# Optimization experiments

Hardware: AMD Instinct MI355X
Metric: run time of the kernel (lower is better)

The kernel has to match this reference:

```python
import jax, jax.numpy as jnp
import numpy as np

WEIGHT = 2e-9       # lambda for the CRF loss
SIGMA_RGB = 15.0    # appearance (color) bandwidth
SIGMA_XY = 100.0    # spatial bandwidth (scaled by SCALE inside the loss, as in the torch module)
SCALE = 0.5         # scale_factor for both image and segmentation


def _nearest_resize(x, sf):
    # torch F.interpolate(mode='nearest'): src_idx = floor(dst_idx / sf)
    H, W = x.shape[-2:]
    Ho, Wo = int(H * sf), int(W * sf)
    iy = jnp.floor(jnp.arange(Ho) / sf).astype(jnp.int32)
    ix = jnp.floor(jnp.arange(Wo) / sf).astype(jnp.int32)
    return x[:, :, iy][:, :, :, ix]


def _bilinear_resize(x, sf):
    # torch F.interpolate(mode='bilinear', align_corners=False): src = (dst+0.5)/sf - 0.5
    N, C, H, W = x.shape
    Ho, Wo = int(H * sf), int(W * sf)

    def axis_idx(n_in, n_out):
        s = (jnp.arange(n_out, dtype=x.dtype) + 0.5) * (n_in / n_out) - 0.5
        s = jnp.clip(s, 0.0, n_in - 1)
        i0 = jnp.floor(s).astype(jnp.int32)
        i1 = jnp.minimum(i0 + 1, n_in - 1)
        w = (s - i0).astype(x.dtype)
        return i0, i1, w

    y0, y1, wy = axis_idx(H, Ho)
    x0, x1, wx = axis_idx(W, Wo)
    xr = x[:, :, y0, :] * (1.0 - wy)[None, None, :, None] + x[:, :, y1, :] * wy[None, None, :, None]
    return xr[:, :, :, x0] * (1.0 - wx) + xr[:, :, :, x1] * wx


def _dense_crf_loss(images, segmentations):
    img = _nearest_resize(images, SCALE)          # [N,3,H,W], values in [0,255]
    seg = _bilinear_resize(segmentations, SCALE)  # [N,K,H,W]
    N, Kc, H, W = seg.shape
    P = H * W
    sxy = SIGMA_XY * SCALE

    yy, xx = jnp.meshgrid(jnp.arange(H, dtype=img.dtype), jnp.arange(W, dtype=img.dtype), indexing='ij')
    pos = jnp.stack([xx, yy], 0) / sxy                       # [2,H,W]
    pos = jnp.broadcast_to(pos[None], (N, 2, H, W))
    feats = jnp.concatenate([pos, img / SIGMA_RGB], axis=1)  # [N,5,H,W]
    feats = feats.reshape(N, 5, P).transpose(0, 2, 1)        # [N,P,5]

    # dense bilateral (Gaussian) kernel: K[p,q] = exp(-||f_p - f_q||^2 / 2)
    sq = jnp.sum(feats * feats, axis=-1)                     # [N,P]
    d2 = sq[:, :, None] + sq[:, None, :] - 2.0 * jnp.einsum('npd,nqd->npq', feats, feats)
    Kmat = jnp.exp(-0.5 * jnp.maximum(d2, 0.0))              # [N,P,P]

    S = seg.reshape(N, Kc, P)                                # [N,K,P]
    AS = jnp.einsum('npq,nkq->nkp', Kmat, S)                 # filtered segmentations
    loss = -jnp.sum(S * AS) / N
    return jnp.reshape(WEIGHT * loss, (1,))


def setup_inputs() -> dict:
    key = jax.random.key(0)
    k1, k2 = jax.random.split(key)
    images = jax.random.uniform(k1, (4, 3, 128, 128), jnp.float32) * 255.0
    logits = jax.random.normal(k2, (4, 2, 128, 128), jnp.float32)
    segmentations = jax.nn.softmax(logits, axis=1)  # softmaxed logits, as per docstring
    return {"images": images, "segmentations": segmentations}


def reference(images, segmentations):
    return _dense_crf_loss(images, segmentations)
```

## Files before the change

kernel.cpp:

```cpp
#include <hip/hip_runtime.h>


#define NIMG 4
#define HW   64
#define PP   (HW * HW)
#define HIN  128
#define MB   4
#define PTILE (256 * MB)
#define QTILE 128
#define NPT  (PP / PTILE)
#define NQT  (PP / QTILE)
#define LOG2E 1.44269504088896f

__global__ __launch_bounds__(256)
void crf_pre(const float* __restrict__ img, const float* __restrict__ seg,
             float4* __restrict__ pts, float* __restrict__ out) {
    int idx = blockIdx.x * 256 + threadIdx.x;
    if (idx == 0) out[0] = 0.0f;
    if (idx >= NIMG * PP) return;
    int n = idx / PP, p = idx % PP;
    int y = p >> 6, x = p & 63;

    const float inv_sxy = 1.0f / 50.0f;
    const float inv_rgb = 1.0f / 15.0f;
    float fx = (float)x * inv_sxy;
    float fy = (float)y * inv_sxy;

    int iy = 2 * y, ix = 2 * x;
    const float* ib = img + (size_t)n * 3 * HIN * HIN;
    float r = ib[(0 * HIN + iy) * HIN + ix] * inv_rgb;
    float g = ib[(1 * HIN + iy) * HIN + ix] * inv_rgb;
    float b = ib[(2 * HIN + iy) * HIN + ix] * inv_rgb;

    const float* sb = seg + (size_t)n * 2 * HIN * HIN;
    float s0, s1;
    {
        const float2* r0 = (const float2*)(sb + (0 * HIN + iy) * HIN + ix);
        const float2* r1 = (const float2*)(sb + (0 * HIN + iy + 1) * HIN + ix);
        float2 a0 = r0[0], a1 = r1[0];
        s0 = 0.25f * ((a0.x + a0.y) + (a1.x + a1.y));
    }
    {
        const float2* r0 = (const float2*)(sb + (1 * HIN + iy) * HIN + ix);
        const float2* r1 = (const float2*)(sb + (1 * HIN + iy + 1) * HIN + ix);
        float2 a0 = r0[0], a1 = r1[0];
        s1 = 0.25f * ((a0.x + a0.y) + (a1.x + a1.y));
    }

    float c0 = -0.5f * LOG2E * (fx * fx + fy * fy + r * r + g * g + b * b);

    float4 v0 = make_float4(fx, fy, r, g);
    float4 v1 = make_float4(b, c0, s0, s1);
    pts[(size_t)idx * 2 + 0] = v0;
    pts[(size_t)idx * 2 + 1] = v1;
}

__global__ __launch_bounds__(256)
void crf_main(const float4* __restrict__ pts, float* __restrict__ out) {
    __shared__ float4 qs[QTILE * 2];
    __shared__ float wsum[4];

    int bid = blockIdx.x;
    int qi = bid % NQT;
    int t  = bid / NQT;
    int pi = t % NPT;
    int n  = t / NPT;

    const float4* src = pts + (size_t)(n * PP + qi * QTILE) * 2;
    qs[threadIdx.x] = src[threadIdx.x];

    float pax[MB], pay[MB], paz[MB], paw[MB], pbx[MB];
    float pc0[MB], ps0[MB], ps1[MB];
    float acc0[MB], acc1[MB];
#pragma unroll
    for (int m = 0; m < MB; ++m) {
        int p = pi * PTILE + m * 256 + threadIdx.x;
        float4 a = pts[(size_t)(n * PP + p) * 2 + 0];
        float4 b = pts[(size_t)(n * PP + p) * 2 + 1];
        pax[m] = a.x * LOG2E; pay[m] = a.y * LOG2E;
        paz[m] = a.z * LOG2E; paw[m] = a.w * LOG2E;
        pbx[m] = b.x * LOG2E;
        pc0[m] = b.y;
        ps0[m] = b.z; ps1[m] = b.w;
        acc0[m] = 0.0f; acc1[m] = 0.0f;
    }
    __syncthreads();

#pragma unroll 2
    for (int q = 0; q < QTILE; ++q) {
        float4 qa = qs[2 * q + 0];
        float4 qb = qs[2 * q + 1];
#pragma unroll
        for (int m = 0; m < MB; ++m) {
            float arg = pc0[m] + qb.y;
            arg = fmaf(pax[m], qa.x, arg);
            arg = fmaf(pay[m], qa.y, arg);
            arg = fmaf(paz[m], qa.z, arg);
            arg = fmaf(paw[m], qa.w, arg);
            arg = fmaf(pbx[m], qb.x, arg);
            float k = __builtin_amdgcn_exp2f(arg);
            acc0[m] = fmaf(k, qb.z, acc0[m]);
            acc1[m] = fmaf(k, qb.w, acc1[m]);
        }
    }

    float acc = 0.0f;
#pragma unroll
    for (int m = 0; m < MB; ++m)
        acc += fmaf(ps0[m], acc0[m], ps1[m] * acc1[m]);

    for (int off = 32; off; off >>= 1) acc += __shfl_down(acc, off, 64);
    if ((threadIdx.x & 63) == 0) wsum[threadIdx.x >> 6] = acc;
    __syncthreads();
    if (threadIdx.x == 0) {
        float s = ((wsum[0] + wsum[1]) + (wsum[2] + wsum[3]));
        atomicAdd(out, s * (-2e-9f / (float)NIMG));
    }
}

extern "C" void kernel_launch(void* const* d_in, const int* in_sizes, int n_in,
                              void* d_out, int out_size, void* d_ws, size_t ws_size,
                              hipStream_t stream) {
    const float* img = (const float*)d_in[0];
    const float* seg = (const float*)d_in[1];
    float* out = (float*)d_out;
    float4* pts = (float4*)d_ws;

    crf_pre<<<(NIMG * PP) / 256, 256, 0, stream>>>(img, seg, pts, out);
    crf_main<<<NIMG * NPT * NQT, 256, 0, stream>>>(pts, out);
}
```

Measured before the change: 78.40 us.

## Exploit kernel symmetry with upper-triangular tiling and fuse preprocessing into main kernel

```diff
diff --git a/kernel.cpp b/kernel.cpp
--- a/kernel.cpp
+++ b/kernel.cpp
@@ -7,20 +7,14 @@
 #define HIN  128
 #define MB   4
 #define PTILE (256 * MB)
-#define QTILE 128
-#define NPT  (PP / PTILE)
-#define NQT  (PP / QTILE)
+#define QTILE 32
 #define LOG2E 1.44269504088896f
 
-__global__ __launch_bounds__(256)
-void crf_pre(const float* __restrict__ img, const float* __restrict__ seg,
-             float4* __restrict__ pts, float* __restrict__ out) {
-    int idx = blockIdx.x * 256 + threadIdx.x;
-    if (idx == 0) out[0] = 0.0f;
-    if (idx >= NIMG * PP) return;
-    int n = idx / PP, p = idx % PP;
+__device__ __forceinline__ void prep_point(const float* __restrict__ img,
+                                           const float* __restrict__ seg,
+                                           int n, int p,
+                                           float4& v0, float4& v1) {
     int y = p >> 6, x = p & 63;
-
     const float inv_sxy = 1.0f / 50.0f;
     const float inv_rgb = 1.0f / 15.0f;
     float fx = (float)x * inv_sxy;
@@ -48,35 +42,47 @@
     }
 
     float c0 = -0.5f * LOG2E * (fx * fx + fy * fy + r * r + g * g + b * b);
-
-    float4 v0 = make_float4(fx, fy, r, g);
-    float4 v1 = make_float4(b, c0, s0, s1);
-    pts[(size_t)idx * 2 + 0] = v0;
-    pts[(size_t)idx * 2 + 1] = v1;
+    v0 = make_float4(fx, fy, r, g);
+    v1 = make_float4(b, c0, s0, s1);
 }
 
 __global__ __launch_bounds__(256)
-void crf_main(const float4* __restrict__ pts, float* __restrict__ out) {
+void crf_fused(const float* __restrict__ img, const float* __restrict__ seg,
+               float* __restrict__ out) {
     __shared__ float4 qs[QTILE * 2];
     __shared__ float wsum[4];
 
     int bid = blockIdx.x;
-    int qi = bid % NQT;
-    int t  = bid / NQT;
-    int pi = t % NPT;
-    int n  = t / NPT;
+    int n = bid / 320;
+    int r = bid - n * 320;
+    int pi, qi;
+    if (r < 128)      { pi = 0; qi = r; }
+    else if (r < 224) { pi = 1; qi = r - 96; }
+    else if (r < 288) { pi = 2; qi = r - 160; }
+    else              { pi = 3; qi = r - 192; }
+    int pbase = pi * PTILE;
+    int qbase = qi * QTILE;
+    bool band = (qbase < pbase + PTILE);
 
-    const float4* src = pts + (size_t)(n * PP + qi * QTILE) * 2;
-    qs[threadIdx.x] = src[threadIdx.x];
+    int tid = threadIdx.x;
+
+    if (tid < QTILE) {
+        float4 v0, v1;
+        prep_point(img, seg, n, qbase + tid, v0, v1);
+        qs[2 * tid + 0] = v0;
+        qs[2 * tid + 1] = v1;
+    }
 
     float pax[MB], pay[MB], paz[MB], paw[MB], pbx[MB];
     float pc0[MB], ps0[MB], ps1[MB];
     float acc0[MB], acc1[MB];
+    int pm[MB];
 #pragma unroll
     for (int m = 0; m < MB; ++m) {
-        int p = pi * PTILE + m * 256 + threadIdx.x;
-        float4 a = pts[(size_t)(n * PP + p) * 2 + 0];
-        float4 b = pts[(size_t)(n * PP + p) * 2 + 1];
+        int p = pbase + m * 256 + tid;
+        pm[m] = p;
+        float4 a, b;
+        prep_point(img, seg, n, p, a, b);
         pax[m] = a.x * LOG2E; pay[m] = a.y * LOG2E;
         paz[m] = a.z * LOG2E; paw[m] = a.w * LOG2E;
         pbx[m] = b.x * LOG2E;
@@ -86,21 +92,43 @@
     }
     __syncthreads();
 
+    if (band) {
 #pragma unroll 2
-    for (int q = 0; q < QTILE; ++q) {
-        float4 qa = qs[2 * q + 0];
-        float4 qb = qs[2 * q + 1];
+        for (int q = 0; q < QTILE; ++q) {
+            float4 qa = qs[2 * q + 0];
+            float4 qb = qs[2 * q + 1];
+            int qg = qbase + q;
 #pragma unroll
-        for (int m = 0; m < MB; ++m) {
-            float arg = pc0[m] + qb.y;
-            arg = fmaf(pax[m], qa.x, arg);
-            arg = fmaf(pay[m], qa.y, arg);
-            arg = fmaf(paz[m], qa.z, arg);
-            arg = fmaf(paw[m], qa.w, arg);
-            arg = fmaf(pbx[m], qb.x, arg);
-            float k = __builtin_amdgcn_exp2f(arg);
-            acc0[m] = fmaf(k, qb.z, acc0[m]);
-            acc1[m] = fmaf(k, qb.w, acc1[m]);
+            for (int m = 0; m < MB; ++m) {
+                float arg = pc0[m] + qb.y;
+                arg = fmaf(pax[m], qa.x, arg);
+                arg = fmaf(pay[m], qa.y, arg);
+                arg = fmaf(paz[m], qa.z, arg);
+                arg = fmaf(paw[m], qa.w, arg);
+                arg = fmaf(pbx[m], qb.x, arg);
+                arg = (qg >= pm[m]) ? arg : -1.0e30f;
+                float k = __builtin_amdgcn_exp2f(arg);
+                acc0[m] = fmaf(k, qb.z, acc0[m]);
+                acc1[m] = fmaf(k, qb.w, acc1[m]);
+            }
+        }
+    } else {
+#pragma unroll 2
+        for (int q = 0; q < QTILE; ++q) {
+            float4 qa = qs[2 * q + 0];
+            float4 qb = qs[2 * q + 1];
+#pragma unroll
+            for (int m = 0; m < MB; ++m) {
+                float arg = pc0[m] + qb.y;
+                arg = fmaf(pax[m], qa.x, arg);
+                arg = fmaf(pay[m], qa.y, arg);
+                arg = fmaf(paz[m], qa.z, arg);
+                arg = fmaf(paw[m], qa.w, arg);
+                arg = fmaf(pbx[m], qb.x, arg);
+                float k = __builtin_amdgcn_exp2f(arg);
+                acc0[m] = fmaf(k, qb.z, acc0[m]);
+                acc1[m] = fmaf(k, qb.w, acc1[m]);
+            }
         }
     }
 
@@ -109,12 +137,21 @@
     for (int m = 0; m < MB; ++m)
         acc += fmaf(ps0[m], acc0[m], ps1[m] * acc1[m]);
 
+    if (band) {
+#pragma unroll
+        for (int m = 0; m < MB; ++m) {
+            bool diag = (pm[m] >= qbase) && (pm[m] < qbase + QTILE);
+            float c = 0.5f * (ps0[m] * ps0[m] + ps1[m] * ps1[m]);
+            acc -= diag ? c : 0.0f;
+        }
+    }
+
     for (int off = 32; off; off >>= 1) acc += __shfl_down(acc, off, 64);
-    if ((threadIdx.x & 63) == 0) wsum[threadIdx.x >> 6] = acc;
+    if ((tid & 63) == 0) wsum[tid >> 6] = acc;
     __syncthreads();
-    if (threadIdx.x == 0) {
+    if (tid == 0) {
         float s = ((wsum[0] + wsum[1]) + (wsum[2] + wsum[3]));
-        atomicAdd(out, s * (-2e-9f / (float)NIMG));
+        atomicAdd(out, s * (-2.0f * 2e-9f / (float)NIMG));
     }
 }
 
@@ -124,8 +161,7 @@
     const float* img = (const float*)d_in[0];
     const float* seg = (const float*)d_in[1];
     float* out = (float*)d_out;
-    float4* pts = (float4*)d_ws;
 
-    crf_pre<<<(NIMG * PP) / 256, 256, 0, stream>>>(img, seg, pts, out);
-    crf_main<<<NIMG * NPT * NQT, 256, 0, stream>>>(pts, out);
+    hipMemsetAsync(out, 0, sizeof(float) * out_size, stream);
+    crf_fused<<<NIMG * 320, 256, 0, stream>>>(img, seg, out);
 }
```

Measured after the change: 78.15 us. About the same (-0.3%).
